# Performance work log

Measured on AMD Instinct MI355X. Metric: run time of the kernel, lower is better.

The kernel has to match this reference:

```python
import jax, jax.numpy as jnp
import numpy as np

N_RAYS = 131072          # rays in batch (e.g., 512x256 tile)
N_SAMPLES = 4194304      # total occupied samples after occ-grid culling (~32/ray)
STEP = 5e-3              # render_step_size (from render_step_size_vals)


def setup_inputs() -> dict:
    key = jax.random.key(0)
    k1, k2, k3, k4 = jax.random.split(key, 4)
    # sorted ray indices, as produced by occGrid.sampling (packed, ascending)
    ray_indices = jnp.sort(jax.random.randint(k1, (N_SAMPLES,), 0, N_RAYS)).astype(jnp.int32)
    t_starts = jax.random.uniform(k2, (N_SAMPLES,), jnp.float32) * 4.0
    t_ends = t_starts + STEP
    sigmas = jax.random.uniform(k3, (N_SAMPLES,), jnp.float32) * 50.0  # raw densities (density_scale=1)
    hdr = jax.random.uniform(k4, (N_SAMPLES, 3), jnp.float32)          # per-sample HDR radiance
    return {"t_starts": t_starts, "t_ends": t_ends, "sigmas": sigmas,
            "hdr": hdr, "ray_indices": ray_indices, "n_rays": N_RAYS}


def _render_and_accumulate(t_starts, t_ends, sigmas, hdr, ray_indices, n_rays):
    S = t_starts.shape[0]
    dt = t_ends - t_starts
    sdt = sigmas * dt                              # sigma * delta_t per sample
    alphas = 1.0 - jnp.exp(-sdt)                   # per-sample alpha
    # exclusive per-ray cumsum of sdt: global exclusive cumsum minus value at segment lead
    excl = jnp.cumsum(sdt) - sdt                   # global exclusive cumsum
    flag = jnp.concatenate([jnp.ones((1,), bool), ray_indices[1:] != ray_indices[:-1]])
    # index of the lead (first) sample of each ray segment, propagated forward
    lead = jax.lax.associative_scan(jnp.maximum, jnp.where(flag, jnp.arange(S), 0))
    trans = jnp.exp(-(excl - excl[lead]))          # transmittance T_i within each ray
    weights = trans * alphas                       # render_weight_from_density
    # accumulate_along_rays (segment reduce); indices are sorted
    opac = jax.ops.segment_sum(weights, ray_indices, num_segments=n_rays,
                               indices_are_sorted=True)                      # [n_rays]
    hdr_acc = jax.ops.segment_sum(weights[:, None] * hdr, ray_indices,
                                  num_segments=n_rays, indices_are_sorted=True)  # [n_rays,3]
    return jnp.concatenate([opac[:, None], hdr_acc], axis=-1)  # [n_rays, 4] = (opacity, hdr)


def reference(t_starts, t_ends, sigmas, hdr, ray_indices, n_rays):
    return _render_and_accumulate(t_starts, t_ends, sigmas, hdr, ray_indices, n_rays)
```

## Files before the change

kernel.cpp:

```cpp
#include <hip/hip_runtime.h>


#define TPB 256
#define LDSF (256 * 17)

#define DPP0(SRC, CTRL, RMASK, BC) __int_as_float(__builtin_amdgcn_update_dpp( \
        0, __float_as_int(SRC), (CTRL), (RMASK), 0xf, (BC)))

#define IMAXD(V, CTRL, RMASK, BC) { \
    int _tmp = __builtin_amdgcn_update_dpp(0, (V), (CTRL), (RMASK), 0xf, (BC)); \
    (V) = ((V) > _tmp) ? (V) : _tmp; }

#define ADD4(A, B) make_float4((A).x + (B).x, (A).y + (B).y, (A).z + (B).z, (A).w + (B).w)

__device__ __forceinline__ float fold16_dpp(float x) {
    float a = 0.0f;
    a = __fadd_rn(a, DPP0(x, 0x110 | 15, 0xf, true));
    a = __fadd_rn(a, DPP0(x, 0x110 | 14, 0xf, true));
    a = __fadd_rn(a, DPP0(x, 0x110 | 13, 0xf, true));
    a = __fadd_rn(a, DPP0(x, 0x110 | 12, 0xf, true));
    a = __fadd_rn(a, DPP0(x, 0x110 | 11, 0xf, true));
    a = __fadd_rn(a, DPP0(x, 0x110 | 10, 0xf, true));
    a = __fadd_rn(a, DPP0(x, 0x110 |  9, 0xf, true));
    a = __fadd_rn(a, DPP0(x, 0x110 |  8, 0xf, true));
    a = __fadd_rn(a, DPP0(x, 0x110 |  7, 0xf, true));
    a = __fadd_rn(a, DPP0(x, 0x110 |  6, 0xf, true));
    a = __fadd_rn(a, DPP0(x, 0x110 |  5, 0xf, true));
    a = __fadd_rn(a, DPP0(x, 0x110 |  4, 0xf, true));
    a = __fadd_rn(a, DPP0(x, 0x110 |  3, 0xf, true));
    a = __fadd_rn(a, DPP0(x, 0x110 |  2, 0xf, true));
    a = __fadd_rn(a, DPP0(x, 0x110 |  1, 0xf, true));
    a = __fadd_rn(a, x);
    return a;
}

__device__ __forceinline__ float wscan(float v) {
    v = __fadd_rn(v, DPP0(v, 0x111, 0xf, true));
    v = __fadd_rn(v, DPP0(v, 0x112, 0xf, true));
    v = __fadd_rn(v, DPP0(v, 0x114, 0xf, true));
    v = __fadd_rn(v, DPP0(v, 0x118, 0xf, true));
    v = __fadd_rn(v, DPP0(v, 0x142, 0xa, false));
    v = __fadd_rn(v, DPP0(v, 0x143, 0xc, false));
    return v;
}

__device__ __forceinline__ float sdt_c(float tsv, float tev, float sgv) {
    return __fmul_rn(sgv, __fsub_rn(tev, tsv));
}

__global__ void k_bottom(const float* __restrict__ ts, const float* __restrict__ te,
                         const float* __restrict__ sg, int S,
                         float* __restrict__ sdt, float* __restrict__ s1,
                         float* __restrict__ T1,
                         float4* __restrict__ out4, int n_rays) {
    __shared__ float lds[LDSF];
    int t = threadIdx.x;
    int tile = blockIdx.x;
    int gid = tile * TPB + t;
    if (gid < n_rays) out4[gid] = make_float4(0.f, 0.f, 0.f, 0.f);
    const float4* ts4 = (const float4*)ts;
    const float4* te4 = (const float4*)te;
    const float4* sg4 = (const float4*)sg;
    float4* sdt4 = (float4*)sdt;
    #pragma unroll
    for (int k = 0; k < 4; ++k) {
        int idx4 = tile * 1024 + k * 256 + t;
        float4 a = ts4[idx4], b = te4[idx4], c = sg4[idx4];
        float4 xo;
        xo.x = sdt_c(a.x, b.x, c.x);
        xo.y = sdt_c(a.y, b.y, c.y);
        xo.z = sdt_c(a.z, b.z, c.z);
        xo.w = sdt_c(a.w, b.w, c.w);
        sdt4[idx4] = xo;
        int fl = (k * 256 + t) << 2;
        int g0 = fl >> 4, j0 = fl & 15;
        float* p = &lds[g0 * 17 + j0];
        p[0] = xo.x; p[1] = xo.y; p[2] = xo.z; p[3] = xo.w;
    }
    __syncthreads();
    float acc = 0.0f;
    #pragma unroll
    for (int j = 0; j < 16; ++j) acc = __fadd_rn(acc, lds[t * 17 + j]);
    float acc2 = fold16_dpp(acc);
    int g = tile * 256 + t;
    s1[g] = acc2;
    if ((t & 15) == 15) T1[g >> 4] = acc2;
}

__global__ void k_mid(const float* __restrict__ T1, float* __restrict__ C2) {
    __shared__ float T2sh[1024];
    __shared__ float s3sh[1024];
    __shared__ float s4sh[64];
    __shared__ float T3sh[64];
    __shared__ float T4sh[4];
    __shared__ float C5sh[4];
    int t = threadIdx.x;
    const float4* T14 = (const float4*)T1;
    float s2l[16];
    float acc = 0.0f;
    #pragma unroll
    for (int k = 0; k < 4; ++k) {
        float4 v = T14[t * 4 + k];
        acc = __fadd_rn(acc, v.x); s2l[k * 4 + 0] = acc;
        acc = __fadd_rn(acc, v.y); s2l[k * 4 + 1] = acc;
        acc = __fadd_rn(acc, v.z); s2l[k * 4 + 2] = acc;
        acc = __fadd_rn(acc, v.w); s2l[k * 4 + 3] = acc;
    }
    T2sh[t] = acc;
    __syncthreads();
    if (t < 64) {
        float a3 = 0.0f;
        for (int j = 0; j < 16; ++j) { a3 = __fadd_rn(a3, T2sh[t * 16 + j]); s3sh[t * 16 + j] = a3; }
        T3sh[t] = a3;
    }
    __syncthreads();
    if (t < 4) {
        float a4 = 0.0f;
        for (int j = 0; j < 16; ++j) { a4 = __fadd_rn(a4, T3sh[t * 16 + j]); s4sh[t * 16 + j] = a4; }
        T4sh[t] = a4;
    }
    __syncthreads();
    if (t == 0) {
        float c = 0.0f;
        for (int r = 0; r < 4; ++r) { c = __fadd_rn(c, T4sh[r]); C5sh[r] = c; }
    }
    __syncthreads();
    if (t < 64) {
        int r = t >> 4;
        float v4 = s4sh[t];
        s4sh[t] = r ? __fadd_rn(v4, C5sh[r - 1]) : v4;
    }
    __syncthreads();
    {
        int r = t >> 4;
        float v3 = s3sh[t];
        float c3 = r ? __fadd_rn(v3, s4sh[r - 1]) : v3;
        s3sh[t] = c3;
    }
    __syncthreads();
    float c3m = t ? s3sh[t - 1] : 0.0f;
    float4* C24 = (float4*)C2;
    #pragma unroll
    for (int k = 0; k < 4; ++k) {
        float4 o;
        o.x = t ? __fadd_rn(s2l[k * 4 + 0], c3m) : s2l[k * 4 + 0];
        o.y = t ? __fadd_rn(s2l[k * 4 + 1], c3m) : s2l[k * 4 + 1];
        o.z = t ? __fadd_rn(s2l[k * 4 + 2], c3m) : s2l[k * 4 + 2];
        o.w = t ? __fadd_rn(s2l[k * 4 + 3], c3m) : s2l[k * 4 + 3];
        C24[t * 4 + k] = o;
    }
}

__global__ void k_render(const int* __restrict__ ri, const float* __restrict__ sdt,
                         const float* __restrict__ s1, const float* __restrict__ C2,
                         const float* __restrict__ hdr,
                         int S, float* __restrict__ out) {
    const int tid = blockIdx.x * TPB + threadIdx.x;
    const int t = threadIdx.x & 63;
    const int i0 = tid * 8;
    const bool valid = i0 < S;

    float4 xa, xb; int4 ra, rb;
    if (valid) {
        xa = ((const float4*)sdt)[2 * tid];
        xb = ((const float4*)sdt)[2 * tid + 1];
        ra = ((const int4*)ri)[2 * tid];
        rb = ((const int4*)ri)[2 * tid + 1];
    } else {
        xa = xb = make_float4(0.f, 0.f, 0.f, 0.f);
        ra.x = ra.y = ra.z = ra.w = -1 - t;
        rb = ra;
    }

    int dpr = __builtin_amdgcn_update_dpp(0, rb.w, 0x111, 0xf, 0xf, true);
    int prev_r = dpr;
    if ((t & 15) == 0) prev_r = (i0 == 0 || !valid) ? (ra.x ^ 1) : ri[i0 - 1];

    bool f0 = prev_r != ra.x;
    bool f1 = ra.y != ra.x, f2 = ra.z != ra.y, f3 = ra.w != ra.z;
    bool f4 = rb.x != ra.w, f5 = rb.y != rb.x, f6 = rb.z != rb.y, f7 = rb.w != rb.z;
    unsigned long long mask0 = __ballot(f0);

    float p0 = __fadd_rn(0.0f, xa.x);
    float p1 = __fadd_rn(p0, xa.y);
    float p2 = __fadd_rn(p1, xa.z);
    float p3 = __fadd_rn(p2, xa.w);
    float p4 = __fadd_rn(p3, xb.x);
    float p5 = __fadd_rn(p4, xb.y);
    float p6 = __fadd_rn(p5, xb.z);
    float p7 = __fadd_rn(p6, xb.w);
    {
        float cin = DPP0(p7, 0x111, 0xf, true);
        float n0 = __fadd_rn(cin, xa.x);
        float n1 = __fadd_rn(n0, xa.y);
        float n2 = __fadd_rn(n1, xa.z);
        float n3 = __fadd_rn(n2, xa.w);
        float n4 = __fadd_rn(n3, xb.x);
        float n5 = __fadd_rn(n4, xb.y);
        float n6 = __fadd_rn(n5, xb.z);
        float n7 = __fadd_rn(n6, xb.w);
        bool me = (t & 1) != 0;
        p0 = me ? n0 : p0; p1 = me ? n1 : p1;
        p2 = me ? n2 : p2; p3 = me ? n3 : p3;
        p4 = me ? n4 : p4; p5 = me ? n5 : p5;
        p6 = me ? n6 : p6; p7 = me ? n7 : p7;
    }

    int g = i0 >> 4;
    float cj = 0.0f;
    if (valid && g) {
        int j3 = g - 1;
        cj = (j3 >> 4) ? __fadd_rn(s1[j3], C2[(j3 >> 4) - 1]) : s1[j3];
    }
    float e0 = __fsub_rn(g ? __fadd_rn(p0, cj) : p0, xa.x);
    float e1 = __fsub_rn(g ? __fadd_rn(p1, cj) : p1, xa.y);
    float e2 = __fsub_rn(g ? __fadd_rn(p2, cj) : p2, xa.z);
    float e3 = __fsub_rn(g ? __fadd_rn(p3, cj) : p3, xa.w);
    float e4 = __fsub_rn(g ? __fadd_rn(p4, cj) : p4, xb.x);
    float e5 = __fsub_rn(g ? __fadd_rn(p5, cj) : p5, xb.y);
    float e6 = __fsub_rn(g ? __fadd_rn(p6, cj) : p6, xb.z);
    float e7 = __fsub_rn(g ? __fadd_rn(p7, cj) : p7, xb.w);

    float el_lead = 0.0f;
    if (!(mask0 & 1ull)) {
        int wbs = (tid - t) * 8;
        int r0v = __builtin_amdgcn_readfirstlane(ra.x);
        int h0 = 0;
        for (int round = 0; round < 65536; ++round) {
            int idx = wbs - 1 - t - 64 * round;
            int rv = (idx >= 0) ? ri[idx] : (r0v ^ 1);
            unsigned long long mm = __ballot(rv != r0v);
            if (mm) {
                int lm = __ffsll((unsigned long long)mm) - 1;
                h0 = wbs - 64 * round - lm;
                break;
            }
        }
        float elv = 0.0f;
        if (t == 0) {
            const float4* s4 = (const float4*)sdt;
            int gh = h0 >> 4, lh = h0 & 15;
            float4 q0 = s4[gh * 4 + 0], q1 = s4[gh * 4 + 1];
            float4 q2 = s4[gh * 4 + 2], q3 = s4[gh * 4 + 3];
            float vv[16] = { q0.x, q0.y, q0.z, q0.w, q1.x, q1.y, q1.z, q1.w,
                             q2.x, q2.y, q2.z, q2.w, q3.x, q3.y, q3.z, q3.w };
            float a2 = 0.0f, xl = 0.0f;
            #pragma unroll
            for (int j2 = 0; j2 < 16; ++j2) {
                if (j2 <= lh) { a2 = __fadd_rn(a2, vv[j2]); xl = vv[j2]; }
            }
            float Ch = a2;
            if (gh) {
                int j3b = gh - 1;
                float cjb = (j3b >> 4) ? __fadd_rn(s1[j3b], C2[(j3b >> 4) - 1]) : s1[j3b];
                Ch = __fadd_rn(a2, cjb);
            }
            elv = __fsub_rn(Ch, xl);
        }
        el_lead = __int_as_float(__builtin_amdgcn_readfirstlane(__float_as_int(elv)));
    }

    bool hb0 = f0, hb1 = f1 | hb0, hb2 = f2 | hb1, hb3 = f3 | hb2;
    bool hb4 = f4 | hb3, hb5 = f5 | hb4, hb6 = f6 | hb5, hb7 = f7 | hb6;

    int key = (valid && hb7) ? (t + 1) : 0;
    int sk = __shfl_up(key, 1, 64);
    if (t == 0) sk = 0;
    int M = sk;
    IMAXD(M, 0x111, 0xf, true)
    IMAXD(M, 0x112, 0xf, true)
    IMAXD(M, 0x114, 0xf, true)
    IMAXD(M, 0x118, 0xf, true)
    IMAXD(M, 0x142, 0xa, false)
    IMAXD(M, 0x143, 0xc, false)
    int src = M;
    int psrc = (src > 0) ? (src - 1) : t;

    float el7c = f7 ? e7 : f6 ? e6 : f5 ? e5 : f4 ? e4 :
                 f3 ? e3 : f2 ? e2 : f1 ? e1 : f0 ? e0 : 0.0f;
    float rel = __shfl(el7c, psrc, 64);
    float el_prev = (src > 0) ? rel : el_lead;

    float el0 = f0 ? e0 : el_prev;
    float el1 = f1 ? e1 : el0;
    float el2 = f2 ? e2 : el1;
    float el3 = f3 ? e3 : el2;
    float el4 = f4 ? e4 : el3;
    float el5 = f5 ? e5 : el4;
    float el6 = f6 ? e6 : el5;
    float el7 = f7 ? e7 : el6;

    float4 h0v, h1v, h2v, h3v, h4v, h5v;
    if (valid) {
        const float4* h4 = (const float4*)hdr;
        h0v = h4[6 * tid + 0]; h1v = h4[6 * tid + 1]; h2v = h4[6 * tid + 2];
        h3v = h4[6 * tid + 3]; h4v = h4[6 * tid + 4]; h5v = h4[6 * tid + 5];
    } else {
        h0v = h1v = h2v = h3v = h4v = h5v = make_float4(0.f, 0.f, 0.f, 0.f);
    }
    float w0 = 0.f, w1 = 0.f, w2 = 0.f, w3 = 0.f;
    float w4 = 0.f, w5 = 0.f, w6 = 0.f, w7 = 0.f;
    if (valid) {
        w0 = __fmul_rn(__expf(-__fsub_rn(e0, el0)), __fsub_rn(1.0f, __expf(-xa.x)));
        w1 = __fmul_rn(__expf(-__fsub_rn(e1, el1)), __fsub_rn(1.0f, __expf(-xa.y)));
        w2 = __fmul_rn(__expf(-__fsub_rn(e2, el2)), __fsub_rn(1.0f, __expf(-xa.z)));
        w3 = __fmul_rn(__expf(-__fsub_rn(e3, el3)), __fsub_rn(1.0f, __expf(-xa.w)));
        w4 = __fmul_rn(__expf(-__fsub_rn(e4, el4)), __fsub_rn(1.0f, __expf(-xb.x)));
        w5 = __fmul_rn(__expf(-__fsub_rn(e5, el5)), __fsub_rn(1.0f, __expf(-xb.y)));
        w6 = __fmul_rn(__expf(-__fsub_rn(e6, el6)), __fsub_rn(1.0f, __expf(-xb.z)));
        w7 = __fmul_rn(__expf(-__fsub_rn(e7, el7)), __fsub_rn(1.0f, __expf(-xb.w)));
    }
    float4 v0 = make_float4(w0, __fmul_rn(w0, h0v.x), __fmul_rn(w0, h0v.y), __fmul_rn(w0, h0v.z));
    float4 v1 = make_float4(w1, __fmul_rn(w1, h0v.w), __fmul_rn(w1, h1v.x), __fmul_rn(w1, h1v.y));
    float4 v2 = make_float4(w2, __fmul_rn(w2, h1v.z), __fmul_rn(w2, h1v.w), __fmul_rn(w2, h2v.x));
    float4 v3 = make_float4(w3, __fmul_rn(w3, h2v.y), __fmul_rn(w3, h2v.z), __fmul_rn(w3, h2v.w));
    float4 v4 = make_float4(w4, __fmul_rn(w4, h3v.x), __fmul_rn(w4, h3v.y), __fmul_rn(w4, h3v.z));
    float4 v5 = make_float4(w5, __fmul_rn(w5, h3v.w), __fmul_rn(w5, h4v.x), __fmul_rn(w5, h4v.y));
    float4 v6 = make_float4(w6, __fmul_rn(w6, h4v.z), __fmul_rn(w6, h4v.w), __fmul_rn(w6, h5v.x));
    float4 v7 = make_float4(w7, __fmul_rn(w7, h5v.y), __fmul_rn(w7, h5v.z), __fmul_rn(w7, h5v.w));

    float4 V0 = v0;
    float4 V1 = ADD4(V0, v1);
    float4 V2 = ADD4(V1, v2);
    float4 V3 = ADD4(V2, v3);
    float4 V4 = ADD4(V3, v4);
    float4 V5 = ADD4(V4, v5);
    float4 V6 = ADD4(V5, v6);
    float4 V7 = ADD4(V6, v7);

    float4 W;
    W.x = wscan(V7.x); W.y = wscan(V7.y); W.z = wscan(V7.z); W.w = wscan(V7.w);
    float4 E;
    E.x = __shfl_up(W.x, 1, 64);
    E.y = __shfl_up(W.y, 1, 64);
    E.z = __shfl_up(W.z, 1, 64);
    E.w = __shfl_up(W.w, 1, 64);
    if (t == 0) { E.x = 0.f; E.y = 0.f; E.z = 0.f; E.w = 0.f; }

    float4 Z = make_float4(0.f, 0.f, 0.f, 0.f);
    float4 B0 = f0 ? E : Z;
    float4 B1 = f1 ? ADD4(E, V0) : B0;
    float4 B2 = f2 ? ADD4(E, V1) : B1;
    float4 B3 = f3 ? ADD4(E, V2) : B2;
    float4 B4 = f4 ? ADD4(E, V3) : B3;
    float4 B5 = f5 ? ADD4(E, V4) : B4;
    float4 B6 = f6 ? ADD4(E, V5) : B5;
    float4 B7 = f7 ? ADD4(E, V6) : B6;

    float4 rbs;
    rbs.x = __shfl(B7.x, psrc, 64);
    rbs.y = __shfl(B7.y, psrc, 64);
    rbs.z = __shfl(B7.z, psrc, 64);
    rbs.w = __shfl(B7.w, psrc, 64);
    float4 bs_prev = (src > 0) ? rbs : Z;

    bool tl0 = f1, tl1 = f2, tl2 = f3, tl3 = f4, tl4 = f5, tl5 = f6, tl6 = f7;
    bool tl7 = (t < 63) ? (((mask0 >> (t + 1)) & 1ull) != 0ull) : true;

#define EMIT(K, TLK, RJ, VK) \
    if (valid && (TLK) && (RJ) >= 0) { \
        float4 bse = hb##K ? B##K : bs_prev; \
        float* o = out + 4 * (RJ); \
        atomicAdd(o + 0, (E.x + (VK).x) - bse.x); \
        atomicAdd(o + 1, (E.y + (VK).y) - bse.y); \
        atomicAdd(o + 2, (E.z + (VK).z) - bse.z); \
        atomicAdd(o + 3, (E.w + (VK).w) - bse.w); \
    }
    EMIT(0, tl0, ra.x, V0)
    EMIT(1, tl1, ra.y, V1)
    EMIT(2, tl2, ra.z, V2)
    EMIT(3, tl3, ra.w, V3)
    EMIT(4, tl4, rb.x, V4)
    EMIT(5, tl5, rb.y, V5)
    EMIT(6, tl6, rb.z, V6)
    EMIT(7, tl7, rb.w, V7)
#undef EMIT
}

extern "C" void kernel_launch(void* const* d_in, const int* in_sizes, int n_in,
                              void* d_out, int out_size, void* d_ws, size_t ws_size,
                              hipStream_t stream) {
    const float* ts  = (const float*)d_in[0];
    const float* te  = (const float*)d_in[1];
    const float* sg  = (const float*)d_in[2];
    const float* hdr = (const float*)d_in[3];
    const int*   ri  = (const int*)d_in[4];
    const int S      = in_sizes[0];
    const int n_rays = out_size / 4;
    const int N1 = S >> 4;
    const int N2 = N1 >> 4;

    char* w = (char*)d_ws;
    auto alloc = [&](size_t bytes) { char* p = w; w += (bytes + 255) & ~255ULL; return p; };
    float* sdt = (float*)alloc((size_t)S * 4);
    float* s1  = (float*)alloc((size_t)N1 * 4);
    float* T1  = (float*)alloc((size_t)N2 * 4);
    float* C2  = (float*)alloc((size_t)N2 * 4);

    k_bottom<<<dim3(N1 / TPB), dim3(TPB), 0, stream>>>(ts, te, sg, S, sdt, s1, T1,
                                                       (float4*)d_out, n_rays);
    k_mid   <<<dim3(1), dim3(1024), 0, stream>>>(T1, C2);
    k_render<<<dim3(S / (TPB * 8)), dim3(TPB), 0, stream>>>(ri, sdt, s1, C2, hdr, S, (float*)d_out);
}
```

Baseline: 167.7 us.

## Fold mid-level scan into last bottom block and process two chunks per render thread

Removes the separate single-block k_mid launch: the last k_bottom block, picked with an atomic ticket and threadfence, computes the block-level prefix sums into C2, staging through a global s2g buffer and reusing the bottom kernel's LDS. The render kernel now handles two 8-sample chunks per thread, loading both sets of inputs up front to overlap memory latency, and launches half as many blocks. This saves one launch and its serial gap, at the cost of a memset for the ticket and a long serial tail in the last bottom block, which runs the whole mid scan with only 256 threads.

```diff
diff --git a/kernel.cpp b/kernel.cpp
--- a/kernel.cpp
+++ b/kernel.cpp
@@ -51,9 +51,11 @@
 __global__ void k_bottom(const float* __restrict__ ts, const float* __restrict__ te,
                          const float* __restrict__ sg, int S,
                          float* __restrict__ sdt, float* __restrict__ s1,
-                         float* __restrict__ T1,
+                         float* __restrict__ T1, float* __restrict__ C2,
+                         float* __restrict__ s2g, int* __restrict__ ticket,
                          float4* __restrict__ out4, int n_rays) {
     __shared__ float lds[LDSF];
+    __shared__ int is_last;
     int t = threadIdx.x;
     int tile = blockIdx.x;
     int gid = tile * TPB + t;
@@ -85,28 +87,36 @@
     int g = tile * 256 + t;
     s1[g] = acc2;
     if ((t & 15) == 15) T1[g >> 4] = acc2;
-}
-
-__global__ void k_mid(const float* __restrict__ T1, float* __restrict__ C2) {
-    __shared__ float T2sh[1024];
-    __shared__ float s3sh[1024];
-    __shared__ float s4sh[64];
-    __shared__ float T3sh[64];
-    __shared__ float T4sh[4];
-    __shared__ float C5sh[4];
-    int t = threadIdx.x;
+
+    __threadfence();
+    if (t == 0) {
+        int old = atomicAdd(ticket, 1);
+        is_last = (old == (int)gridDim.x - 1);
+    }
+    __syncthreads();
+    if (!is_last) return;
+    __threadfence();
+
+    float* T2sh = lds;
+    float* s3sh = lds + 1024;
+    float* s4sh = lds + 2048;
+    float* T3sh = lds + 2112;
+    float* T4sh = lds + 2176;
+    float* C5sh = lds + 2180;
     const float4* T14 = (const float4*)T1;
-    float s2l[16];
-    float acc = 0.0f;
-    #pragma unroll
-    for (int k = 0; k < 4; ++k) {
-        float4 v = T14[t * 4 + k];
-        acc = __fadd_rn(acc, v.x); s2l[k * 4 + 0] = acc;
-        acc = __fadd_rn(acc, v.y); s2l[k * 4 + 1] = acc;
-        acc = __fadd_rn(acc, v.z); s2l[k * 4 + 2] = acc;
-        acc = __fadd_rn(acc, v.w); s2l[k * 4 + 3] = acc;
-    }
-    T2sh[t] = acc;
+    for (int q = 0; q < 4; ++q) {
+        int grp = t + 256 * q;
+        float a2 = 0.0f;
+        #pragma unroll
+        for (int kk = 0; kk < 4; ++kk) {
+            float4 v = T14[grp * 4 + kk];
+            a2 = __fadd_rn(a2, v.x); s2g[grp * 16 + kk * 4 + 0] = a2;
+            a2 = __fadd_rn(a2, v.y); s2g[grp * 16 + kk * 4 + 1] = a2;
+            a2 = __fadd_rn(a2, v.z); s2g[grp * 16 + kk * 4 + 2] = a2;
+            a2 = __fadd_rn(a2, v.w); s2g[grp * 16 + kk * 4 + 3] = a2;
+        }
+        T2sh[grp] = a2;
+    }
     __syncthreads();
     if (t < 64) {
         float a3 = 0.0f;
@@ -131,50 +141,32 @@
         s4sh[t] = r ? __fadd_rn(v4, C5sh[r - 1]) : v4;
     }
     __syncthreads();
-    {
-        int r = t >> 4;
-        float v3 = s3sh[t];
-        float c3 = r ? __fadd_rn(v3, s4sh[r - 1]) : v3;
-        s3sh[t] = c3;
-    }
-    __syncthreads();
-    float c3m = t ? s3sh[t - 1] : 0.0f;
-    float4* C24 = (float4*)C2;
-    #pragma unroll
-    for (int k = 0; k < 4; ++k) {
-        float4 o;
-        o.x = t ? __fadd_rn(s2l[k * 4 + 0], c3m) : s2l[k * 4 + 0];
-        o.y = t ? __fadd_rn(s2l[k * 4 + 1], c3m) : s2l[k * 4 + 1];
-        o.z = t ? __fadd_rn(s2l[k * 4 + 2], c3m) : s2l[k * 4 + 2];
-        o.w = t ? __fadd_rn(s2l[k * 4 + 3], c3m) : s2l[k * 4 + 3];
-        C24[t * 4 + k] = o;
-    }
-}
-
-__global__ void k_render(const int* __restrict__ ri, const float* __restrict__ sdt,
-                         const float* __restrict__ s1, const float* __restrict__ C2,
-                         const float* __restrict__ hdr,
-                         int S, float* __restrict__ out) {
-    const int tid = blockIdx.x * TPB + threadIdx.x;
-    const int t = threadIdx.x & 63;
+    for (int e = t; e < 1024; e += 256) {
+        int r = e >> 4;
+        float v3 = s3sh[e];
+        s3sh[e] = r ? __fadd_rn(v3, s4sh[r - 1]) : v3;
+    }
+    __syncthreads();
+    for (int j = t; j < 16384; j += 256) {
+        int gq = j >> 4;
+        float v = s2g[j];
+        C2[j] = gq ? __fadd_rn(v, s3sh[gq - 1]) : v;
+    }
+}
+
+__device__ __forceinline__ void render_chunk(
+    int tid, int t, int S,
+    float4 xa, float4 xb, int4 ra, int4 rb, int prb, float cj,
+    const int* __restrict__ ri, const float* __restrict__ sdt,
+    const float* __restrict__ s1, const float* __restrict__ C2,
+    const float* __restrict__ hdr, float* __restrict__ out)
+{
     const int i0 = tid * 8;
     const bool valid = i0 < S;
 
-    float4 xa, xb; int4 ra, rb;
-    if (valid) {
-        xa = ((const float4*)sdt)[2 * tid];
-        xb = ((const float4*)sdt)[2 * tid + 1];
-        ra = ((const int4*)ri)[2 * tid];
-        rb = ((const int4*)ri)[2 * tid + 1];
-    } else {
-        xa = xb = make_float4(0.f, 0.f, 0.f, 0.f);
-        ra.x = ra.y = ra.z = ra.w = -1 - t;
-        rb = ra;
-    }
-
     int dpr = __builtin_amdgcn_update_dpp(0, rb.w, 0x111, 0xf, 0xf, true);
     int prev_r = dpr;
-    if ((t & 15) == 0) prev_r = (i0 == 0 || !valid) ? (ra.x ^ 1) : ri[i0 - 1];
+    if ((t & 15) == 0) prev_r = (i0 == 0 || !valid) ? (ra.x ^ 1) : prb;
 
     bool f0 = prev_r != ra.x;
     bool f1 = ra.y != ra.x, f2 = ra.z != ra.y, f3 = ra.w != ra.z;
@@ -207,11 +199,6 @@
     }
 
     int g = i0 >> 4;
-    float cj = 0.0f;
-    if (valid && g) {
-        int j3 = g - 1;
-        cj = (j3 >> 4) ? __fadd_rn(s1[j3], C2[(j3 >> 4) - 1]) : s1[j3];
-    }
     float e0 = __fsub_rn(g ? __fadd_rn(p0, cj) : p0, xa.x);
     float e1 = __fsub_rn(g ? __fadd_rn(p1, cj) : p1, xa.y);
     float e2 = __fsub_rn(g ? __fadd_rn(p2, cj) : p2, xa.z);
@@ -377,6 +364,49 @@
 #undef EMIT
 }
 
+__global__ void k_render(const int* __restrict__ ri, const float* __restrict__ sdt,
+                         const float* __restrict__ s1, const float* __restrict__ C2,
+                         const float* __restrict__ hdr,
+                         int S, float* __restrict__ out) {
+    const int t = threadIdx.x & 63;
+    const int TOT = S >> 4;
+    const int tidA = blockIdx.x * TPB + threadIdx.x;
+    const int tidB = tidA + TOT;
+
+    float4 xaA = ((const float4*)sdt)[2 * tidA];
+    float4 xbA = ((const float4*)sdt)[2 * tidA + 1];
+    int4  raA = ((const int4*)ri)[2 * tidA];
+    int4  rbA = ((const int4*)ri)[2 * tidA + 1];
+    float4 xaB = ((const float4*)sdt)[2 * tidB];
+    float4 xbB = ((const float4*)sdt)[2 * tidB + 1];
+    int4  raB = ((const int4*)ri)[2 * tidB];
+    int4  rbB = ((const int4*)ri)[2 * tidB + 1];
+
+    int prbA = 0, prbB = 0;
+    if ((t & 15) == 0) {
+        int iA = tidA * 8, iB = tidB * 8;
+        if (iA > 0) prbA = ri[iA - 1];
+        prbB = ri[iB - 1];
+    }
+
+    float cjA = 0.0f, cjB = 0.0f;
+    {
+        int jA = (tidA >> 1) - 1;
+        if (jA >= 0) {
+            float s1v = s1[jA];
+            cjA = (jA >> 4) ? __fadd_rn(s1v, C2[(jA >> 4) - 1]) : s1v;
+        }
+        int jB = (tidB >> 1) - 1;
+        float s1w = s1[jB];
+        cjB = (jB >> 4) ? __fadd_rn(s1w, C2[(jB >> 4) - 1]) : s1w;
+    }
+
+    render_chunk(tidA, t, S, xaA, xbA, raA, rbA, prbA, cjA,
+                 ri, sdt, s1, C2, hdr, out);
+    render_chunk(tidB, t, S, xaB, xbB, raB, rbB, prbB, cjB,
+                 ri, sdt, s1, C2, hdr, out);
+}
+
 extern "C" void kernel_launch(void* const* d_in, const int* in_sizes, int n_in,
                               void* d_out, int out_size, void* d_ws, size_t ws_size,
                               hipStream_t stream) {
@@ -396,9 +426,13 @@
     float* s1  = (float*)alloc((size_t)N1 * 4);
     float* T1  = (float*)alloc((size_t)N2 * 4);
     float* C2  = (float*)alloc((size_t)N2 * 4);
-
+    float* s2g = (float*)alloc((size_t)N2 * 4);
+    int* ticket = (int*)alloc(256);
+
+    hipMemsetAsync(ticket, 0, 4, stream);
     k_bottom<<<dim3(N1 / TPB), dim3(TPB), 0, stream>>>(ts, te, sg, S, sdt, s1, T1,
+                                                       C2, s2g, ticket,
                                                        (float4*)d_out, n_rays);
-    k_mid   <<<dim3(1), dim3(1024), 0, stream>>>(T1, C2);
-    k_render<<<dim3(S / (TPB * 8)), dim3(TPB), 0, stream>>>(ri, sdt, s1, C2, hdr, S, (float*)d_out);
-}
+    k_render<<<dim3(S / (TPB * 16)), dim3(TPB), 0, stream>>>(ri, sdt, s1, C2, hdr,
+                                                             S, (float*)d_out);
+}
```

Result: slower. 343.5 us (+104.9%).
